# Performance work log

Measured on AMD Instinct MI355X. Metric: run time of the kernel, lower is better.

Reference implementation:

```python
import jax, jax.numpy as jnp
import numpy as np

B, T, E, H = 2, 2048, 1024, 16
D = E // H  # head_dim = 64


def setup_inputs() -> dict:
    key = jax.random.key(0)
    ks = jax.random.split(key, 7)
    s = 1.0 / np.sqrt(E)
    queries = jax.random.normal(ks[0], (B, T, E), dtype=jnp.float32)
    keys = jax.random.normal(ks[1], (B, T, E), dtype=jnp.float32)
    values = jax.random.normal(ks[2], (B, T, E), dtype=jnp.float32)
    # causal mask: True where attention is disallowed (masked_fill semantics)
    mask = jnp.triu(jnp.ones((T, T), dtype=bool), k=1)[None, None]  # [1,1,T,T]
    Wq = jax.random.uniform(ks[3], (E, E), jnp.float32, -s, s)
    Wk = jax.random.uniform(ks[4], (E, E), jnp.float32, -s, s)
    Wv = jax.random.uniform(ks[5], (E, E), jnp.float32, -s, s)
    Wo = jax.random.uniform(ks[6], (E, E), jnp.float32, -s, s)
    return {"queries": queries, "keys": keys, "values": values, "mask": mask,
            "Wq": Wq, "Wk": Wk, "Wv": Wv, "Wo": Wo}


def _split(x):
    # [B,T,E] -> [B,H,T,D]
    return x.reshape(B, T, H, D).transpose(0, 2, 1, 3)


def reference(queries, keys, values, mask, Wq, Wk, Wv, Wo):
    # nn.Linear(E,E,bias=False): y = x @ W.T
    q = _split(queries @ Wq.T)  # [B,H,T,D]
    k = _split(keys @ Wk.T)
    v = _split(values @ Wv.T)
    scores = jnp.einsum('bhqd,bhkd->bhqk', q, k) / jnp.sqrt(jnp.float32(D))
    scores = jnp.where(mask, -jnp.inf, scores)
    weights = jax.nn.softmax(scores, axis=-1)
    attn = jnp.einsum('bhqk,bhkd->bhqd', weights, v)  # [B,H,T,D]
    joined = attn.transpose(0, 2, 1, 3).reshape(B, T, E)
    return joined @ Wo.T
```

## Files before the change

### kernel.cpp

```cpp
#include <hip/hip_runtime.h>
#include <hip/hip_bf16.h>

#define T_DIM 2048
#define E_DIM 1024
#define MM 4096
#define NN 1024
#define KK 1024

typedef __attribute__((ext_vector_type(8))) short bh8;
typedef __attribute__((ext_vector_type(4))) short bh4;
typedef __attribute__((ext_vector_type(4))) float fx4;

static __device__ __forceinline__ short f2bf(float f) {
  union { float f; unsigned u; } v; v.f = f;
  unsigned r = (v.u + 0x7fffu + ((v.u >> 16) & 1u)) >> 16;
  return (short)(unsigned short)r;
}

static __device__ __forceinline__ void gload16(const void* g, void* l) {
  __builtin_amdgcn_global_load_lds(
      (const __attribute__((address_space(1))) unsigned*)g,
      (__attribute__((address_space(3))) unsigned*)l, 16, 0, 0);
}

__global__ __launch_bounds__(256) void cvt_w(const float* __restrict__ s0,
                                             const float* __restrict__ s1,
                                             const float* __restrict__ s2,
                                             const float* __restrict__ s3,
                                             short* __restrict__ dst) {
  int a = blockIdx.y;
  const float* sp = a == 0 ? s0 : a == 1 ? s1 : a == 2 ? s2 : s3;
  size_t i = ((size_t)blockIdx.x * 256 + threadIdx.x) * 8;
  fx4 x = *(const fx4*)(sp + i);
  fx4 y = *(const fx4*)(sp + i + 4);
  bh8 o;
#pragma unroll
  for (int j = 0; j < 4; j++) { o[j] = f2bf(x[j]); o[4 + j] = f2bf(y[j]); }
  *(bh8*)(dst + (size_t)a * (NN * KK) + i) = o;
}

template<bool AF32, bool OUTF32>
__global__ __launch_bounds__(256) void gemm_fast(const void* __restrict__ A0,
                                                 const void* __restrict__ A1,
                                                 const void* __restrict__ A2,
                                                 const short* __restrict__ W0,
                                                 void* __restrict__ C0)
{
  __shared__ short As[128 * 32];
  __shared__ short Bs[128 * 32];
  const int tid = threadIdx.x;
  const int lane = tid & 63, w = tid >> 6;
  const int lm = lane & 15, lg = lane >> 4;
  const int wr = w >> 1, wc = w & 1;
  const int m0 = blockIdx.y * 128, n0 = blockIdx.x * 128;
  const int z = blockIdx.z;
  const void* Ap = z == 0 ? A0 : z == 1 ? A1 : A2;
  const short* W = W0 + (size_t)z * (NN * KK);

  fx4 acc[4][4] = {};

  for (int k0 = 0; k0 < KK; k0 += 32) {
    __syncthreads();
#pragma unroll
    for (int c = 0; c < 2; c++) {
      int idx = c * 256 + tid;
      int row = idx >> 2, kc = idx & 3;
      gload16(W + (size_t)(n0 + row) * KK + k0 + kc * 8, Bs + idx * 8);
      if constexpr (AF32) {
        const float* Af = (const float*)Ap;
        const float* src = Af + (size_t)(m0 + row) * KK + k0 + kc * 8;
        fx4 x = *(const fx4*)src;
        fx4 y = *(const fx4*)(src + 4);
        bh8 o;
#pragma unroll
        for (int j = 0; j < 4; j++) { o[j] = f2bf(x[j]); o[4 + j] = f2bf(y[j]); }
        *(bh8*)&As[idx * 8] = o;
      } else {
        const short* Ab = (const short*)Ap;
        gload16(Ab + (size_t)(m0 + row) * KK + k0 + kc * 8, As + idx * 8);
      }
    }
    __syncthreads();
    bh8 af[4], bf[4];
#pragma unroll
    for (int mi = 0; mi < 4; mi++)
      af[mi] = *(const bh8*)&As[(wr * 64 + mi * 16 + lm) * 32 + lg * 8];
#pragma unroll
    for (int ni = 0; ni < 4; ni++)
      bf[ni] = *(const bh8*)&Bs[(wc * 64 + ni * 16 + lm) * 32 + lg * 8];
#pragma unroll
    for (int mi = 0; mi < 4; mi++)
#pragma unroll
      for (int ni = 0; ni < 4; ni++)
        acc[mi][ni] = __builtin_amdgcn_mfma_f32_16x16x32_bf16(af[mi], bf[ni], acc[mi][ni], 0, 0, 0);
  }

#pragma unroll
  for (int mi = 0; mi < 4; mi++)
#pragma unroll
    for (int ni = 0; ni < 4; ni++) {
      int row = m0 + wr * 64 + mi * 16 + lg * 4;
      int col = n0 + wc * 64 + ni * 16 + lm;
#pragma unroll
      for (int r = 0; r < 4; r++) {
        float vv = acc[mi][ni][r];
        if constexpr (OUTF32) ((float*)C0)[(size_t)z * MM * NN + (size_t)(row + r) * NN + col] = vv;
        else ((short*)C0)[(size_t)z * MM * NN + (size_t)(row + r) * NN + col] = f2bf(vv);
      }
    }
}

template<bool AF32, bool OUTF32>
__global__ __launch_bounds__(256) void gemm_nt(const void* __restrict__ Ap,
                                               const float* __restrict__ Bw,
                                               void* __restrict__ Cp,
                                               int M, int N, int K)
{
  __shared__ short As[128 * 40];
  __shared__ short Bs[128 * 40];
  const int tid = threadIdx.x;
  const int lane = tid & 63;
  const int w = tid >> 6;
  const int lm = lane & 15;
  const int lg = lane >> 4;
  const int wr = w >> 1, wc = w & 1;
  const int m0 = blockIdx.y * 128, n0 = blockIdx.x * 128;

  fx4 acc[4][4] = {};

  for (int k0 = 0; k0 < K; k0 += 32) {
    __syncthreads();
#pragma unroll
    for (int i = 0; i < 4; ++i) {
      int g = i * 256 + tid;
      int row = g >> 3, cg = g & 7;
      bh4 a4;
      if constexpr (AF32) {
        const float* A = (const float*)Ap;
        fx4 v = *(const fx4*)(A + (size_t)(m0 + row) * K + k0 + cg * 4);
#pragma unroll
        for (int j = 0; j < 4; j++) a4[j] = f2bf(v[j]);
      } else {
        const short* A = (const short*)Ap;
        a4 = *(const bh4*)(A + (size_t)(m0 + row) * K + k0 + cg * 4);
      }
      *(bh4*)&As[row * 40 + cg * 4] = a4;

      fx4 bv = *(const fx4*)(Bw + (size_t)(n0 + row) * K + k0 + cg * 4);
      bh4 b4;
#pragma unroll
      for (int j = 0; j < 4; j++) b4[j] = f2bf(bv[j]);
      *(bh4*)&Bs[row * 40 + cg * 4] = b4;
    }
    __syncthreads();

    bh8 af[4], bf[4];
#pragma unroll
    for (int mi = 0; mi < 4; mi++)
      af[mi] = *(const bh8*)&As[(wr * 64 + mi * 16 + lm) * 40 + lg * 8];
#pragma unroll
    for (int ni = 0; ni < 4; ni++)
      bf[ni] = *(const bh8*)&Bs[(wc * 64 + ni * 16 + lm) * 40 + lg * 8];
#pragma unroll
    for (int mi = 0; mi < 4; mi++)
#pragma unroll
      for (int ni = 0; ni < 4; ni++)
        acc[mi][ni] = __builtin_amdgcn_mfma_f32_16x16x32_bf16(af[mi], bf[ni], acc[mi][ni], 0, 0, 0);
  }

#pragma unroll
  for (int mi = 0; mi < 4; mi++) {
#pragma unroll
    for (int ni = 0; ni < 4; ni++) {
      int row = m0 + wr * 64 + mi * 16 + lg * 4;
      int col = n0 + wc * 64 + ni * 16 + lm;
#pragma unroll
      for (int r = 0; r < 4; r++) {
        float vv = acc[mi][ni][r];
        if constexpr (OUTF32) ((float*)Cp)[(size_t)(row + r) * N + col] = vv;
        else        ((short*)Cp)[(size_t)(row + r) * N + col] = f2bf(vv);
      }
    }
  }
}

__global__ __launch_bounds__(256) void attn_kernel(const short* __restrict__ Q,
                                                   const short* __restrict__ Kb,
                                                   const short* __restrict__ Vb,
                                                   short* __restrict__ At)
{
  __shared__ short Kl[64 * 64];
  __shared__ short Vt[64 * 64];
  __shared__ short Pl[4 * 16 * 72];

  const int tid = threadIdx.x;
  const int lane = tid & 63;
  const int w = tid >> 6;
  const int lm = lane & 15;
  const int lg = lane >> 4;
  const int pi = blockIdx.x;
  const int bh = blockIdx.y;
  const size_t headoff = (size_t)(bh >> 4) * T_DIM * E_DIM + (size_t)(bh & 15) * 64;

  for (int s = 0; s < 2; s++) {
    const int qt = s ? (31 - pi) : pi;
    const int q0 = qt * 64;

    const int qrow = q0 + w * 16 + lm;
    bh8 qf[2];
#pragma unroll
    for (int ks = 0; ks < 2; ks++)
      qf[ks] = *(const bh8*)(Q + headoff + (size_t)qrow * E_DIM + ks * 32 + lg * 8);

    fx4 oacc[4] = {};
    float m_r[4], l_r[4];
#pragma unroll
    for (int r = 0; r < 4; r++) { m_r[r] = -INFINITY; l_r[r] = 0.0f; }

    for (int t = 0; t <= qt; ++t) {
      const int kv0 = t * 64;
      __syncthreads();
#pragma unroll
      for (int c = 0; c < 2; c++) {
        int idx = c * 256 + tid;
        int row = idx >> 3, ch = idx & 7;
        gload16(Kb + headoff + (size_t)(kv0 + row) * E_DIM + ((ch ^ (row & 7)) * 8),
                Kl + idx * 8);
      }
      bh8 v8[2];
#pragma unroll
      for (int c = 0; c < 2; c++) {
        int idx = c * 256 + tid;
        int row = idx >> 3, ch = idx & 7;
        v8[c] = *(const bh8*)(Vb + headoff + (size_t)(kv0 + row) * E_DIM + ch * 8);
      }
#pragma unroll
      for (int c = 0; c < 2; c++) {
        int idx = c * 256 + tid;
        int row = idx >> 3, ch = idx & 7;
#pragma unroll
        for (int j = 0; j < 8; j++) {
          int d = ch * 8 + j;
          Vt[d * 64 + (((row >> 3) ^ ((ch + j) & 7)) * 8) + (row & 7)] = v8[c][j];
        }
      }
      __syncthreads();

      fx4 sacc[4] = {};
#pragma unroll
      for (int nb = 0; nb < 4; nb++) {
        const int rK = nb * 16 + lm;
#pragma unroll
        for (int ks = 0; ks < 2; ks++) {
          bh8 kf = *(const bh8*)&Kl[rK * 64 + (((ks * 4 + lg) ^ (lm & 7)) * 8)];
          sacc[nb] = __builtin_amdgcn_mfma_f32_16x16x32_bf16(qf[ks], kf, sacc[nb], 0, 0, 0);
        }
      }

      float sv[4][4];
      const bool maskt = (t == qt);
#pragma unroll
      for (int nb = 0; nb < 4; nb++)
#pragma unroll
        for (int r = 0; r < 4; r++) {
          float x = sacc[nb][r] * 0.125f;
          if (maskt && (nb * 16 + lm > w * 16 + lg * 4 + r)) x = -INFINITY;
          sv[nb][r] = x;
        }

      float p[4][4];
#pragma unroll
      for (int r = 0; r < 4; r++) {
        float rm = fmaxf(fmaxf(sv[0][r], sv[1][r]), fmaxf(sv[2][r], sv[3][r]));
#pragma unroll
        for (int off = 1; off < 16; off <<= 1) rm = fmaxf(rm, __shfl_xor(rm, off));
        float mn = fmaxf(m_r[r], rm);
        float fac = __expf(m_r[r] - mn);
        float ps = 0.0f;
#pragma unroll
        for (int nb = 0; nb < 4; nb++) { p[nb][r] = __expf(sv[nb][r] - mn); ps += p[nb][r]; }
#pragma unroll
        for (int off = 1; off < 16; off <<= 1) ps += __shfl_xor(ps, off);
        l_r[r] = l_r[r] * fac + ps;
        m_r[r] = mn;
#pragma unroll
        for (int db = 0; db < 4; db++) oacc[db][r] *= fac;
      }

#pragma unroll
      for (int nb = 0; nb < 4; nb++)
#pragma unroll
        for (int r = 0; r < 4; r++)
          Pl[w * 1152 + (lg * 4 + r) * 72 + nb * 16 + lm] = f2bf(p[nb][r]);

      bh8 pa[2];
#pragma unroll
      for (int ks = 0; ks < 2; ks++)
        pa[ks] = *(const bh8*)&Pl[w * 1152 + lm * 72 + ks * 32 + lg * 8];
#pragma unroll
      for (int db = 0; db < 4; db++) {
        const int d = db * 16 + lm;
        const int gsw = ((d >> 3) + (d & 7)) & 7;
#pragma unroll
        for (int ks = 0; ks < 2; ks++) {
          bh8 vf = *(const bh8*)&Vt[d * 64 + (((ks * 4 + lg) ^ gsw) * 8)];
          oacc[db] = __builtin_amdgcn_mfma_f32_16x16x32_bf16(pa[ks], vf, oacc[db], 0, 0, 0);
        }
      }
    }

#pragma unroll
    for (int r = 0; r < 4; r++) {
      float rl = 1.0f / l_r[r];
      int row = q0 + w * 16 + lg * 4 + r;
#pragma unroll
      for (int db = 0; db < 4; db++)
        At[headoff + (size_t)row * E_DIM + db * 16 + lm] = f2bf(oacc[db][r] * rl);
    }
  }
}

extern "C" void kernel_launch(void* const* d_in, const int* in_sizes, int n_in,
                              void* d_out, int out_size, void* d_ws, size_t ws_size,
                              hipStream_t stream)
{
  const float* q  = (const float*)d_in[0];
  const float* k  = (const float*)d_in[1];
  const float* v  = (const float*)d_in[2];
  const float* Wq = (const float*)d_in[4];
  const float* Wk = (const float*)d_in[5];
  const float* Wv = (const float*)d_in[6];
  const float* Wo = (const float*)d_in[7];

  short* Qb  = (short*)d_ws;
  short* Kb  = Qb + (size_t)MM * NN;
  short* Vb  = Kb + (size_t)MM * NN;
  short* At  = Vb + (size_t)MM * NN;
  short* wqb = At + (size_t)MM * NN;

  const size_t need_fast = ((size_t)4 * MM * NN + (size_t)4 * NN * KK) * 2;
  if (ws_size >= need_fast) {
    cvt_w<<<dim3(NN * KK / (256 * 8), 4), 256, 0, stream>>>(Wq, Wk, Wv, Wo, wqb);
    gemm_fast<true, false><<<dim3(NN / 128, MM / 128, 3), 256, 0, stream>>>(q, k, v, wqb, Qb);
    attn_kernel<<<dim3(16, 32), 256, 0, stream>>>(Qb, Kb, Vb, At);
    gemm_fast<false, true><<<dim3(NN / 128, MM / 128, 1), 256, 0, stream>>>(At, At, At, wqb + (size_t)3 * NN * KK, d_out);
  } else {
    dim3 gg(NN / 128, MM / 128);
    gemm_nt<true, false><<<gg, 256, 0, stream>>>(q, Wq, Qb, MM, NN, KK);
    gemm_nt<true, false><<<gg, 256, 0, stream>>>(k, Wk, Kb, MM, NN, KK);
    gemm_nt<true, false><<<gg, 256, 0, stream>>>(v, Wv, Vb, MM, NN, KK);
    attn_kernel<<<dim3(16, 32), 256, 0, stream>>>(Qb, Kb, Vb, At);
    gemm_nt<false, true><<<gg, 256, 0, stream>>>(At, Wo, d_out, MM, NN, KK);
  }
}
```

Measured before the change: 278.1 us.

## Double-buffer K/V tiles in attention and pre-convert activations to bf16

The attention kernel now keeps two K/V shared-memory buffers. It prefetches the next tile's K via async global-to-LDS loads and V into registers while the current tile computes, which removes one barrier per iteration. When the workspace is large enough, a separate pass first converts the fp32 Q/K/V activations to bf16, so the projection GEMM can use the bf16 A path instead of converting inline. The trade-off is double the LDS for K/V, more register pressure from the prefetched V, and an extra pass over the activations.

```diff
diff --git a/kernel.cpp b/kernel.cpp
--- a/kernel.cpp
+++ b/kernel.cpp
@@ -6,6 +6,8 @@
 #define MM 4096
 #define NN 1024
 #define KK 1024
+#define MSZ ((size_t)MM * KK)
+#define WSZ ((size_t)NN * KK)
 
 typedef __attribute__((ext_vector_type(8))) short bh8;
 typedef __attribute__((ext_vector_type(4))) short bh4;
@@ -36,7 +38,22 @@
   bh8 o;
 #pragma unroll
   for (int j = 0; j < 4; j++) { o[j] = f2bf(x[j]); o[4 + j] = f2bf(y[j]); }
-  *(bh8*)(dst + (size_t)a * (NN * KK) + i) = o;
+  *(bh8*)(dst + (size_t)a * WSZ + i) = o;
+}
+
+__global__ __launch_bounds__(256) void cvt_act(const float* __restrict__ s0,
+                                               const float* __restrict__ s1,
+                                               const float* __restrict__ s2,
+                                               short* __restrict__ dst) {
+  int a = blockIdx.y;
+  const float* sp = a == 0 ? s0 : a == 1 ? s1 : s2;
+  size_t i = ((size_t)blockIdx.x * 256 + threadIdx.x) * 8;
+  fx4 x = *(const fx4*)(sp + i);
+  fx4 y = *(const fx4*)(sp + i + 4);
+  bh8 o;
+#pragma unroll
+  for (int j = 0; j < 4; j++) { o[j] = f2bf(x[j]); o[4 + j] = f2bf(y[j]); }
+  *(bh8*)(dst + (size_t)a * MSZ + i) = o;
 }
 
 template<bool AF32, bool OUTF32>
@@ -55,7 +72,7 @@
   const int m0 = blockIdx.y * 128, n0 = blockIdx.x * 128;
   const int z = blockIdx.z;
   const void* Ap = z == 0 ? A0 : z == 1 ? A1 : A2;
-  const short* W = W0 + (size_t)z * (NN * KK);
+  const short* W = W0 + (size_t)z * WSZ;
 
   fx4 acc[4][4] = {};
 
@@ -104,8 +121,8 @@
 #pragma unroll
       for (int r = 0; r < 4; r++) {
         float vv = acc[mi][ni][r];
-        if constexpr (OUTF32) ((float*)C0)[(size_t)z * MM * NN + (size_t)(row + r) * NN + col] = vv;
-        else ((short*)C0)[(size_t)z * MM * NN + (size_t)(row + r) * NN + col] = f2bf(vv);
+        if constexpr (OUTF32) ((float*)C0)[(size_t)z * MSZ + (size_t)(row + r) * NN + col] = vv;
+        else ((short*)C0)[(size_t)z * MSZ + (size_t)(row + r) * NN + col] = f2bf(vv);
       }
     }
 }
@@ -189,8 +206,8 @@
                                                    const short* __restrict__ Vb,
                                                    short* __restrict__ At)
 {
-  __shared__ short Kl[64 * 64];
-  __shared__ short Vt[64 * 64];
+  __shared__ short Kl[2][64 * 64];
+  __shared__ short Vt[2][64 * 64];
   __shared__ short Pl[4 * 16 * 72];
 
   const int tid = threadIdx.x;
@@ -202,6 +219,9 @@
   const int bh = blockIdx.y;
   const size_t headoff = (size_t)(bh >> 4) * T_DIM * E_DIM + (size_t)(bh & 15) * 64;
 
+  const int r0 = tid >> 3, ch0 = tid & 7;
+  const int r1 = (256 + tid) >> 3, ch1 = tid & 7;
+
   for (int s = 0; s < 2; s++) {
     const int qt = s ? (31 - pi) : pi;
     const int q0 = qt * 64;
@@ -217,34 +237,33 @@
 #pragma unroll
     for (int r = 0; r < 4; r++) { m_r[r] = -INFINITY; l_r[r] = 0.0f; }
 
+    {
+      gload16(Kb + headoff + (size_t)r0 * E_DIM + ((ch0 ^ (r0 & 7)) * 8), &Kl[0][tid * 8]);
+      gload16(Kb + headoff + (size_t)r1 * E_DIM + ((ch1 ^ (r1 & 7)) * 8), &Kl[0][(256 + tid) * 8]);
+      bh8 v8a = *(const bh8*)(Vb + headoff + (size_t)r0 * E_DIM + ch0 * 8);
+      bh8 v8b = *(const bh8*)(Vb + headoff + (size_t)r1 * E_DIM + ch1 * 8);
+#pragma unroll
+      for (int j = 0; j < 8; j++) {
+        int d = ch0 * 8 + j;
+        Vt[0][d * 64 + (((r0 >> 3) ^ ((ch0 + j) & 7)) * 8) + (r0 & 7)] = v8a[j];
+        Vt[0][d * 64 + (((r1 >> 3) ^ ((ch1 + j) & 7)) * 8) + (r1 & 7)] = v8b[j];
+      }
+    }
+    __syncthreads();
+
+    int cur = 0;
     for (int t = 0; t <= qt; ++t) {
-      const int kv0 = t * 64;
-      __syncthreads();
-#pragma unroll
-      for (int c = 0; c < 2; c++) {
-        int idx = c * 256 + tid;
-        int row = idx >> 3, ch = idx & 7;
-        gload16(Kb + headoff + (size_t)(kv0 + row) * E_DIM + ((ch ^ (row & 7)) * 8),
-                Kl + idx * 8);
-      }
-      bh8 v8[2];
-#pragma unroll
-      for (int c = 0; c < 2; c++) {
-        int idx = c * 256 + tid;
-        int row = idx >> 3, ch = idx & 7;
-        v8[c] = *(const bh8*)(Vb + headoff + (size_t)(kv0 + row) * E_DIM + ch * 8);
-      }
-#pragma unroll
-      for (int c = 0; c < 2; c++) {
-        int idx = c * 256 + tid;
-        int row = idx >> 3, ch = idx & 7;
-#pragma unroll
-        for (int j = 0; j < 8; j++) {
-          int d = ch * 8 + j;
-          Vt[d * 64 + (((row >> 3) ^ ((ch + j) & 7)) * 8) + (row & 7)] = v8[c][j];
-        }
-      }
-      __syncthreads();
+      const bool pre = (t < qt);
+      bh8 v8a, v8b;
+      if (pre) {
+        const int kvn = (t + 1) * 64;
+        gload16(Kb + headoff + (size_t)(kvn + r0) * E_DIM + ((ch0 ^ (r0 & 7)) * 8),
+                &Kl[cur ^ 1][tid * 8]);
+        gload16(Kb + headoff + (size_t)(kvn + r1) * E_DIM + ((ch1 ^ (r1 & 7)) * 8),
+                &Kl[cur ^ 1][(256 + tid) * 8]);
+        v8a = *(const bh8*)(Vb + headoff + (size_t)(kvn + r0) * E_DIM + ch0 * 8);
+        v8b = *(const bh8*)(Vb + headoff + (size_t)(kvn + r1) * E_DIM + ch1 * 8);
+      }
 
       fx4 sacc[4] = {};
 #pragma unroll
@@ -252,7 +271,7 @@
         const int rK = nb * 16 + lm;
 #pragma unroll
         for (int ks = 0; ks < 2; ks++) {
-          bh8 kf = *(const bh8*)&Kl[rK * 64 + (((ks * 4 + lg) ^ (lm & 7)) * 8)];
+          bh8 kf = *(const bh8*)&Kl[cur][rK * 64 + (((ks * 4 + lg) ^ (lm & 7)) * 8)];
           sacc[nb] = __builtin_amdgcn_mfma_f32_16x16x32_bf16(qf[ks], kf, sacc[nb], 0, 0, 0);
         }
       }
@@ -303,10 +322,21 @@
         const int gsw = ((d >> 3) + (d & 7)) & 7;
 #pragma unroll
         for (int ks = 0; ks < 2; ks++) {
-          bh8 vf = *(const bh8*)&Vt[d * 64 + (((ks * 4 + lg) ^ gsw) * 8)];
+          bh8 vf = *(const bh8*)&Vt[cur][d * 64 + (((ks * 4 + lg) ^ gsw) * 8)];
           oacc[db] = __builtin_amdgcn_mfma_f32_16x16x32_bf16(pa[ks], vf, oacc[db], 0, 0, 0);
         }
       }
+
+      if (pre) {
+#pragma unroll
+        for (int j = 0; j < 8; j++) {
+          int d = ch0 * 8 + j;
+          Vt[cur ^ 1][d * 64 + (((r0 >> 3) ^ ((ch0 + j) & 7)) * 8) + (r0 & 7)] = v8a[j];
+          Vt[cur ^ 1][d * 64 + (((r1 >> 3) ^ ((ch1 + j) & 7)) * 8) + (r1 & 7)] = v8b[j];
+        }
+      }
+      __syncthreads();
+      cur ^= 1;
     }
 
 #pragma unroll
@@ -333,23 +363,38 @@
   const float* Wo = (const float*)d_in[7];
 
   short* Qb  = (short*)d_ws;
-  short* Kb  = Qb + (size_t)MM * NN;
-  short* Vb  = Kb + (size_t)MM * NN;
-  short* At  = Vb + (size_t)MM * NN;
-  short* wqb = At + (size_t)MM * NN;
-
-  const size_t need_fast = ((size_t)4 * MM * NN + (size_t)4 * NN * KK) * 2;
-  if (ws_size >= need_fast) {
-    cvt_w<<<dim3(NN * KK / (256 * 8), 4), 256, 0, stream>>>(Wq, Wk, Wv, Wo, wqb);
-    gemm_fast<true, false><<<dim3(NN / 128, MM / 128, 3), 256, 0, stream>>>(q, k, v, wqb, Qb);
-    attn_kernel<<<dim3(16, 32), 256, 0, stream>>>(Qb, Kb, Vb, At);
-    gemm_fast<false, true><<<dim3(NN / 128, MM / 128, 1), 256, 0, stream>>>(At, At, At, wqb + (size_t)3 * NN * KK, d_out);
+  short* Kbb = Qb + MSZ;
+  short* Vbb = Kbb + MSZ;
+  short* wqb = Vbb + MSZ;
+  short* Xq  = wqb + 4 * WSZ;
+  short* At  = Xq;
+
+  const size_t need_full = (3 * MSZ + 4 * WSZ + 3 * MSZ) * 2;
+  const size_t need_mid  = (4 * MSZ + 4 * WSZ) * 2;
+
+  if (ws_size >= need_full) {
+    cvt_act<<<dim3(MSZ / (256 * 8), 3), 256, 0, stream>>>(q, k, v, Xq);
+    cvt_w<<<dim3(WSZ / (256 * 8), 4), 256, 0, stream>>>(Wq, Wk, Wv, Wo, wqb);
+    gemm_fast<false, false><<<dim3(NN / 128, MM / 128, 3), 256, 0, stream>>>(
+        Xq, Xq + MSZ, Xq + 2 * MSZ, wqb, Qb);
+    attn_kernel<<<dim3(16, 32), 256, 0, stream>>>(Qb, Kbb, Vbb, At);
+    gemm_fast<false, true><<<dim3(NN / 128, MM / 128, 1), 256, 0, stream>>>(
+        At, At, At, wqb + 3 * WSZ, d_out);
+  } else if (ws_size >= need_mid) {
+    short* At2  = Vbb + MSZ;
+    short* wqb2 = At2 + MSZ;
+    cvt_w<<<dim3(WSZ / (256 * 8), 4), 256, 0, stream>>>(Wq, Wk, Wv, Wo, wqb2);
+    gemm_fast<true, false><<<dim3(NN / 128, MM / 128, 3), 256, 0, stream>>>(q, k, v, wqb2, Qb);
+    attn_kernel<<<dim3(16, 32), 256, 0, stream>>>(Qb, Kbb, Vbb, At2);
+    gemm_fast<false, true><<<dim3(NN / 128, MM / 128, 1), 256, 0, stream>>>(
+        At2, At2, At2, wqb2 + 3 * WSZ, d_out);
   } else {
+    short* At2 = Vbb + MSZ;
     dim3 gg(NN / 128, MM / 128);
     gemm_nt<true, false><<<gg, 256, 0, stream>>>(q, Wq, Qb, MM, NN, KK);
-    gemm_nt<true, false><<<gg, 256, 0, stream>>>(k, Wk, Kb, MM, NN, KK);
-    gemm_nt<true, false><<<gg, 256, 0, stream>>>(v, Wv, Vb, MM, NN, KK);
-    attn_kernel<<<dim3(16, 32), 256, 0, stream>>>(Qb, Kb, Vb, At);
-    gemm_nt<false, true><<<gg, 256, 0, stream>>>(At, Wo, d_out, MM, NN, KK);
+    gemm_nt<true, false><<<gg, 256, 0, stream>>>(k, Wk, Kbb, MM, NN, KK);
+    gemm_nt<true, false><<<gg, 256, 0, stream>>>(v, Wv, Vbb, MM, NN, KK);
+    attn_kernel<<<dim3(16, 32), 256, 0, stream>>>(Qb, Kbb, Vbb, At2);
+    gemm_nt<false, true><<<gg, 256, 0, stream>>>(At2, Wo, d_out, MM, NN, KK);
   }
 }
```

New measurement: 262.8 us. 1.06x faster.
